# Performance work log

Measured on AMD Instinct MI355X. Metric: run time of the kernel, lower is better.

## Reference

```python
import jax, jax.numpy as jnp
import numpy as np

N_IN, M_MID = 512, 256
B, H, W = 16, 64, 64

def setup_inputs() -> dict:
    key = jax.random.key(0)
    ks = jax.random.split(key, 7)
    s = 0.05
    return {
        "x": jax.random.normal(ks[0], (B, N_IN, H, W), dtype=jnp.float32),
        "W_state": jax.random.normal(ks[1], (M_MID, N_IN), dtype=jnp.float32) * s,
        "b_state": jax.random.normal(ks[2], (M_MID,), dtype=jnp.float32) * s,
        "W_proj": jax.random.normal(ks[3], (M_MID, N_IN), dtype=jnp.float32) * s,
        "b_proj": jax.random.normal(ks[4], (M_MID,), dtype=jnp.float32) * s,
        "W_extend": jax.random.normal(ks[5], (N_IN, M_MID), dtype=jnp.float32) * s,
        "b_extend": jax.random.normal(ks[6], (N_IN,), dtype=jnp.float32) * s,
    }

def reference(x, W_state, b_state, W_proj, b_proj, W_extend, b_extend):
    n, c, h, w = x.shape
    hw = h * w
    xf = x.reshape(n, c, hw)                                   # [n, C, HW]
    # 1x1 convs are channel GEMMs over flattened spatial dim
    x_state = jnp.einsum('mc,nch->nmh', W_state, xf) + b_state[None, :, None]   # [n, M, HW]
    x_proj = jnp.einsum('mc,nch->nmh', W_proj, xf) + b_proj[None, :, None]      # [n, M, HW]
    # bmm -> scale -> softmax -> bmm (graph reasoning over M x M)
    scores = jnp.einsum('nmh,nkh->nmk', x_state, x_proj) / jnp.sqrt(jnp.float32(hw))
    attn = jax.nn.softmax(scores, axis=2)                      # [n, M, M]
    x_rstate = jnp.einsum('nmk,nkh->nmh', attn, x_proj)        # [n, M, HW]
    # extend back to C channels + residual
    ext = jnp.einsum('cm,nmh->nch', W_extend, x_rstate) + b_extend[None, :, None]
    return x + ext.reshape(n, c, h, w)
```

## Files before the change

### kernel.cpp

```cpp
#include <hip/hip_runtime.h>
#include <hip/hip_bf16.h>
#include <stdint.h>

typedef __bf16 bf16x8_t __attribute__((ext_vector_type(8)));
typedef float  f32x4_t  __attribute__((ext_vector_type(4)));
typedef short  short8_t __attribute__((ext_vector_type(8)));

__device__ __forceinline__ unsigned short f2b(float f) {
    union { float f; unsigned u; } v; v.f = f;
    unsigned u = v.u;
    return (unsigned short)((u + 0x7FFFu + ((u >> 16) & 1u)) >> 16);
}
__device__ __forceinline__ float b2f(unsigned short b) {
    union { unsigned u; float f; } v; v.u = ((unsigned)b) << 16; return v.f;
}

#define AS3(p) ((__attribute__((address_space(3))) void*)(p))
#define AS1(p) ((const __attribute__((address_space(1))) void*)(p))
#define FENCE() asm volatile("" ::: "memory")

#define NB   16
#define CIN  512
#define MMID 256
#define HW   4096
#define KSPLIT 4
#define ASZ  (128 * 64)
#define ASZA (512 * 64)
#define ASZB (128 * 64)

__device__ __forceinline__ void swz3(int gx, int gy, int& bx, int& by, int& bz) {
    const int nwg = gridDim.x, ord = blockIdx.x, q = nwg >> 3;
    const int s = (ord & 7) * q + (ord >> 3);
    by = s % gy;
    const int rem = s / gy;
    bx = rem % gx;
    bz = rem / gx;
}

__global__ __launch_bounds__(256) void prep_weights(
    const float* __restrict__ Ws, const float* __restrict__ Wp,
    const float* __restrict__ Wef, const float* __restrict__ bs,
    const float* __restrict__ bp,
    unsigned short* __restrict__ Wsp, unsigned short* __restrict__ Wex,
    unsigned short* __restrict__ WpT, float* __restrict__ bsp)
{
    int i = blockIdx.x * 256 + threadIdx.x;
    if (i < MMID * CIN) {
        Wsp[i]              = f2b(Ws[i]);
        Wsp[MMID * CIN + i] = f2b(Wp[i]);
        Wex[i]              = f2b(Wef[i]);
        const int c = i >> 8, k = i & (MMID - 1);
        WpT[i] = f2b(Wp[(size_t)k * CIN + c]);
    }
    if (i < MMID) { bsp[i] = bs[i]; bsp[MMID + i] = bp[i]; }
}

__global__ __launch_bounds__(256) void transpose_convert_x(
    const float* __restrict__ x, unsigned short* __restrict__ xT)
{
    __shared__ unsigned short tile[64][66];
    const int n = blockIdx.z, c0 = blockIdx.y * 64, h0 = blockIdx.x * 64;
    const float* s = x + ((size_t)n * CIN + c0) * HW + h0;
    unsigned short* d = xT + ((size_t)n * HW + h0) * CIN + c0;
    const int t = threadIdx.x;
    {
        const int rr = t >> 4, cc = (t & 15) * 4;
        #pragma unroll
        for (int p = 0; p < 4; ++p) {
            int r = p * 16 + rr;
            float4 v = *(const float4*)(s + (size_t)r * HW + cc);
            tile[r][cc + 0] = f2b(v.x); tile[r][cc + 1] = f2b(v.y);
            tile[r][cc + 2] = f2b(v.z); tile[r][cc + 3] = f2b(v.w);
        }
    }
    __syncthreads();
    {
        const int wr = t >> 3, wc = (t & 7) * 8;
        #pragma unroll
        for (int p = 0; p < 2; ++p) {
            int h = p * 32 + wr;
            unsigned short tmp[8];
            #pragma unroll
            for (int j = 0; j < 8; ++j) tmp[j] = tile[wc + j][h];
            *(short8_t*)(d + (size_t)h * CIN + wc) = *(const short8_t*)tmp;
        }
    }
}

__global__ __launch_bounds__(256) void transpose_bf16_64(
    const unsigned short* __restrict__ src, unsigned short* __restrict__ dst,
    int srs, int drs, long long sbs, long long dbs)
{
    __shared__ unsigned short tile[64][66];
    const int n = blockIdx.z, r0 = blockIdx.y * 64, c0 = blockIdx.x * 64;
    const unsigned short* s = src + (size_t)n * sbs + (size_t)r0 * srs + c0;
    unsigned short* d = dst + (size_t)n * dbs + (size_t)c0 * drs + r0;
    const int t = threadIdx.x;
    const int rr = t >> 3, cc = (t & 7) * 8;
    #pragma unroll
    for (int p = 0; p < 2; ++p) {
        int r = p * 32 + rr;
        short8_t v = *(const short8_t*)(s + (size_t)r * srs + cc);
        #pragma unroll
        for (int j = 0; j < 8; ++j) tile[r][cc + j] = ((const unsigned short*)&v)[j];
    }
    __syncthreads();
    #pragma unroll
    for (int p = 0; p < 2; ++p) {
        int c = p * 32 + rr;
        unsigned short tmp[8];
        #pragma unroll
        for (int j = 0; j < 8; ++j) tmp[j] = tile[cc + j][c];
        *(short8_t*)(d + (size_t)c * drs + cc) = *(const short8_t*)tmp;
    }
}

template <int EPI>
__device__ __forceinline__ void epilogue_repack(
    f32x4_t (&acc)[4][4], unsigned short* smem,
    int m0, int n0, int wave, int lane,
    void* __restrict__ Cout, int ldc, size_t cbase)
{
    float* fbuf = (float*)smem;
    const int t   = wave * 64 + lane;
    const int l15 = lane & 15, l16 = lane >> 4;
    const int wr2 = wave >> 1;
    const int wc  = (wave & 1) * 64;

    #pragma unroll
    for (int p = 0; p < 4; ++p) {
        __syncthreads();
        if (wr2 == (p >> 1)) {
            const int ihalf = p & 1;
            #pragma unroll
            for (int i2 = 0; i2 < 2; ++i2) {
                const int i = ihalf * 2 + i2;
                #pragma unroll
                for (int r = 0; r < 4; ++r) {
                    const int lrow = i2 * 16 + l16 * 4 + r;
                    #pragma unroll
                    for (int j = 0; j < 4; ++j)
                        fbuf[lrow * 132 + wc + j * 16 + l15] = acc[i][j][r];
                }
            }
        }
        __syncthreads();
        #pragma unroll
        for (int it = 0; it < 2; ++it) {
            const int lrow = it * 16 + (t >> 4);
            const int col  = (t & 15) * 8;
            const int row  = m0 + p * 32 + lrow;
            float v[8];
            *(float4*)&v[0] = *(const float4*)&fbuf[lrow * 132 + col];
            *(float4*)&v[4] = *(const float4*)&fbuf[lrow * 132 + col + 4];
            const size_t idx = cbase + (size_t)row * ldc + n0 + col;
            if constexpr (EPI == 1) {
                float* op = (float*)Cout + idx;
                *(float4*)op = *(const float4*)&v[0];
                *(float4*)(op + 4) = *(const float4*)&v[4];
            } else if constexpr (EPI == 4) {
                unsigned short o[8];
                #pragma unroll
                for (int k = 0; k < 8; ++k)
                    o[k] = f2b(v[k] + ((row == n0 + col + k) ? 1.0f : 0.0f));
                *(short8_t*)((unsigned short*)Cout + idx) = *(const short8_t*)o;
            } else {
                unsigned short o[8];
                #pragma unroll
                for (int k = 0; k < 8; ++k) o[k] = f2b(v[k]);
                *(short8_t*)((unsigned short*)Cout + idx) = *(const short8_t*)o;
            }
        }
    }
}

#define GEMM_KLOOP(Ab, Bb, lda, ldb, KBEG, NT)                                          \
    auto stage = [&](int k0, int b) {                                                   \
        unsigned short* Asb = smem + b * 2 * ASZ;                                       \
        unsigned short* Bsb = Asb + ASZ;                                                \
        _Pragma("unroll")                                                               \
        for (int c = 0; c < 4; ++c) {                                                   \
            const int o   = (c * 256 + t) * 16;                                         \
            const int row = o >> 7;                                                     \
            const int ce  = ((o & 127) ^ ((row & 7) << 4)) >> 1;                        \
            __builtin_amdgcn_global_load_lds(                                           \
                AS1(Ab + (size_t)row * lda + k0 + ce), AS3((char*)Asb + o), 16, 0, 0);  \
            __builtin_amdgcn_global_load_lds(                                           \
                AS1(Bb + (size_t)row * ldb + k0 + ce), AS3((char*)Bsb + o), 16, 0, 0);  \
        }                                                                               \
    };                                                                                  \
    stage(KBEG, 0);                                                                     \
    for (int itk = 0; itk < (NT); ++itk) {                                              \
        const int cur = itk & 1;                                                        \
        if (itk + 1 < (NT)) {                                                           \
            stage(KBEG + (itk + 1) * 64, cur ^ 1);                                      \
            asm volatile("s_waitcnt vmcnt(8)" ::: "memory");                            \
        } else {                                                                        \
            asm volatile("s_waitcnt vmcnt(0)" ::: "memory");                            \
        }                                                                               \
        __builtin_amdgcn_s_barrier();                                                   \
        FENCE();                                                                        \
        const char* Asb = (const char*)(smem + cur * 2 * ASZ);                          \
        const char* Bsb = Asb + 2 * ASZ;                                                \
        const int swz = (l15 & 7) << 4;                                                 \
        _Pragma("unroll")                                                               \
        for (int ks = 0; ks < 2; ++ks) {                                                \
            bf16x8_t af[4], bfr[4];                                                     \
            const int cb = (ks * 64 + l16 * 16) ^ swz;                                  \
            _Pragma("unroll")                                                           \
            for (int i = 0; i < 4; ++i) {                                               \
                af[i]  = *(const bf16x8_t*)(Asb + (wr + i * 16 + l15) * 128 + cb);      \
                bfr[i] = *(const bf16x8_t*)(Bsb + (wc + i * 16 + l15) * 128 + cb);      \
            }                                                                           \
            _Pragma("unroll")                                                           \
            for (int i = 0; i < 4; ++i)                                                 \
                _Pragma("unroll")                                                       \
                for (int j = 0; j < 4; ++j)                                             \
                    acc[i][j] = __builtin_amdgcn_mfma_f32_16x16x32_bf16(                \
                        af[i], bfr[j], acc[i][j], 0, 0, 0);                             \
        }                                                                               \
        FENCE();                                                                        \
        __builtin_amdgcn_s_barrier();                                                   \
        FENCE();                                                                        \
    }

template <int EPI>
__global__ __launch_bounds__(512, 1) void gemm512(
    const unsigned short* __restrict__ A, const unsigned short* __restrict__ B,
    long long strideA, long long strideB,
    const float* __restrict__ bias, int bias_bstride,
    void* __restrict__ Cout, int ldc, long long strideC, int gx)
{
    __shared__ unsigned short smem[2 * (ASZA + ASZB)];

    int bx, by, n;  swz3(gx, 1, bx, by, n);
    const int n0 = bx * 128;

    const unsigned short* Ab = A + (size_t)n * strideA;
    const unsigned short* Bb = B + (size_t)n * strideB + (size_t)n0 * CIN;

    const int t    = threadIdx.x;
    const int lane = t & 63;
    const int wave = t >> 6;
    const int wr   = (wave >> 1) * 128;
    const int wc   = (wave & 1) * 64;
    const int l15  = lane & 15;
    const int l16  = lane >> 4;

    f32x4_t acc[8][4] = {};

    auto stage = [&](int k0, int b) {
        unsigned short* Asb = smem + b * (ASZA + ASZB);
        unsigned short* Bsb = Asb + ASZA;
        #pragma unroll
        for (int c = 0; c < 8; ++c) {
            const int o   = (c * 512 + t) * 16;
            const int row = o >> 7;
            const int ce  = ((o & 127) ^ ((row & 7) << 4)) >> 1;
            __builtin_amdgcn_global_load_lds(
                AS1(Ab + (size_t)row * CIN + k0 + ce), AS3((char*)Asb + o), 16, 0, 0);
        }
        #pragma unroll
        for (int c = 0; c < 2; ++c) {
            const int o   = (c * 512 + t) * 16;
            const int row = o >> 7;
            const int ce  = ((o & 127) ^ ((row & 7) << 4)) >> 1;
            __builtin_amdgcn_global_load_lds(
                AS1(Bb + (size_t)row * CIN + k0 + ce), AS3((char*)Bsb + o), 16, 0, 0);
        }
    };

    const int NT = CIN / 64;
    stage(0, 0);
    for (int itk = 0; itk < NT; ++itk) {
        const int cur = itk & 1;
        if (itk + 1 < NT) {
            stage((itk + 1) * 64, cur ^ 1);
            asm volatile("s_waitcnt vmcnt(10)" ::: "memory");
        } else {
            asm volatile("s_waitcnt vmcnt(0)" ::: "memory");
        }
        __builtin_amdgcn_s_barrier();
        FENCE();
        const char* Asb = (const char*)(smem + cur * (ASZA + ASZB));
        const char* Bsb = Asb + 2 * ASZA;
        const int swz = (l15 & 7) << 4;
        #pragma unroll
        for (int ks = 0; ks < 2; ++ks) {
            const int cb = (ks * 64 + l16 * 16) ^ swz;
            bf16x8_t af[8], bfr[4];
            #pragma unroll
            for (int i = 0; i < 8; ++i)
                af[i] = *(const bf16x8_t*)(Asb + (wr + i * 16 + l15) * 128 + cb);
            #pragma unroll
            for (int j = 0; j < 4; ++j)
                bfr[j] = *(const bf16x8_t*)(Bsb + (wc + j * 16 + l15) * 128 + cb);
            #pragma unroll
            for (int i = 0; i < 8; ++i)
                #pragma unroll
                for (int j = 0; j < 4; ++j)
                    acc[i][j] = __builtin_amdgcn_mfma_f32_16x16x32_bf16(
                        af[i], bfr[j], acc[i][j], 0, 0, 0);
        }
        FENCE();
        __builtin_amdgcn_s_barrier();
        FENCE();
    }

    float* fbuf = (float*)smem;
    const size_t cbase = (size_t)n * strideC;
    const float* beff = bias + (size_t)n * bias_bstride;
    #pragma unroll
    for (int p = 0; p < 16; ++p) {
        __syncthreads();
        if ((wave >> 1) == (p >> 2)) {
            #pragma unroll
            for (int i2 = 0; i2 < 2; ++i2) {
                const int i = (p & 3) * 2 + i2;
                #pragma unroll
                for (int r = 0; r < 4; ++r) {
                    const int lrow = i2 * 16 + l16 * 4 + r;
                    #pragma unroll
                    for (int j = 0; j < 4; ++j)
                        fbuf[lrow * 132 + wc + j * 16 + l15] = acc[i][j][r];
                }
            }
        }
        __syncthreads();
        const int lrow = t >> 4;
        const int col  = (t & 15) * 8;
        const int row  = p * 32 + lrow;
        float v[8];
        *(float4*)&v[0] = *(const float4*)&fbuf[lrow * 132 + col];
        *(float4*)&v[4] = *(const float4*)&fbuf[lrow * 132 + col + 4];
        const float badd = beff[row];
        const size_t idx = cbase + (size_t)row * ldc + n0 + col;
        if constexpr (EPI == 1) {
            float o[8];
            #pragma unroll
            for (int k = 0; k < 8; ++k) o[k] = v[k] + badd;
            float* op = (float*)Cout + idx;
            *(float4*)op = *(const float4*)&o[0];
            *(float4*)(op + 4) = *(const float4*)&o[4];
        } else {
            unsigned short o[8];
            #pragma unroll
            for (int k = 0; k < 8; ++k) o[k] = f2b(v[k] + badd);
            *(short8_t*)((unsigned short*)Cout + idx) = *(const short8_t*)o;
        }
    }
}

__global__ __launch_bounds__(256) void gemm_scores(
    const unsigned short* __restrict__ Ysp, float* __restrict__ scoresP)
{
    __shared__ unsigned short smem[4 * ASZ];

    int bx, by, z;  swz3(MMID / 128, MMID / 128, bx, by, z);
    const int n  = z >> 2;
    const int kc = z & 3;
    const int m0 = by * 128;
    const int n0 = bx * 128;

    const unsigned short* Ab = Ysp + (size_t)n * CIN * HW + (size_t)m0 * HW;
    const unsigned short* Bb = Ysp + (size_t)n * CIN * HW + (size_t)(MMID + n0) * HW;

    const int t    = threadIdx.x;
    const int lane = t & 63;
    const int wave = t >> 6;
    const int wr   = (wave >> 1) * 64;
    const int wc   = (wave & 1) * 64;
    const int l15  = lane & 15;
    const int l16  = lane >> 4;

    f32x4_t acc[4][4] = {};
    const int kbeg = kc * (HW / KSPLIT);
    GEMM_KLOOP(Ab, Bb, HW, HW, kbeg, (HW / KSPLIT) / 64)

    float* outp = scoresP + (size_t)(kc * NB + n) * MMID * MMID;
    epilogue_repack<1>(acc, smem, m0, n0, wave, lane, outp, MMID, 0);
}

__global__ __launch_bounds__(256) void softmax_rows(
    const float* __restrict__ scoresP, unsigned short* __restrict__ attn)
{
    const int wave = threadIdx.x >> 6;
    const int l    = threadIdx.x & 63;
    const size_t row = (size_t)blockIdx.x * 4 + wave;
    const size_t pstride = (size_t)NB * MMID * MMID;
    float4 v = {0.f, 0.f, 0.f, 0.f};
    #pragma unroll
    for (int p = 0; p < KSPLIT; ++p) {
        float4 u = *(const float4*)(scoresP + p * pstride + row * MMID + l * 4);
        v.x += u.x; v.y += u.y; v.z += u.z; v.w += u.w;
    }
    float mx = fmaxf(fmaxf(v.x, v.y), fmaxf(v.z, v.w));
    #pragma unroll
    for (int off = 32; off; off >>= 1) mx = fmaxf(mx, __shfl_xor(mx, off));
    const float sc = 0.015625f;
    float e0 = __expf((v.x - mx) * sc), e1 = __expf((v.y - mx) * sc);
    float e2 = __expf((v.z - mx) * sc), e3 = __expf((v.w - mx) * sc);
    float sum = e0 + e1 + e2 + e3;
    #pragma unroll
    for (int off = 32; off; off >>= 1) sum += __shfl_xor(sum, off);
    const float inv = 1.0f / sum;
    unsigned short o[4] = { f2b(e0 * inv), f2b(e1 * inv), f2b(e2 * inv), f2b(e3 * inv) };
    *(uint64_t*)(attn + row * MMID + l * 4) = *(const uint64_t*)o;
}

__global__ __launch_bounds__(256) void compute_vec(
    const unsigned short* __restrict__ G, const float* __restrict__ bsp,
    const float* __restrict__ be, float* __restrict__ vec)
{
    const int n = blockIdx.x >> 1;
    const int c = ((blockIdx.x & 1) << 8) + threadIdx.x;
    const unsigned short* g = G + ((size_t)n * CIN + c) * MMID;
    float s = 0.f;
    for (int k = 0; k < MMID; k += 8) {
        short8_t v = *(const short8_t*)(g + k);
        #pragma unroll
        for (int j = 0; j < 8; ++j)
            s += b2f((unsigned short)v[j]) * bsp[MMID + k + j];
    }
    vec[n * CIN + c] = be[c] + s;
}

template <int EPI>
__global__ __launch_bounds__(256) void gemm_nt(
    const unsigned short* __restrict__ A, const unsigned short* __restrict__ B,
    int lda, int ldb, int K,
    long long strideA, long long strideB,
    void* __restrict__ Cout, int ldc, long long strideC,
    int gx, int gy)
{
    __shared__ unsigned short smem[4 * ASZ];

    int bx, by, n;  swz3(gx, gy, bx, by, n);
    const int m0 = by * 128;
    const int n0 = bx * 128;

    const unsigned short* Ab = A + (size_t)n * strideA + (size_t)m0 * lda;
    const unsigned short* Bb = B + (size_t)n * strideB + (size_t)n0 * ldb;

    const int t    = threadIdx.x;
    const int lane = t & 63;
    const int wave = t >> 6;
    const int wr   = (wave >> 1) * 64;
    const int wc   = (wave & 1) * 64;
    const int l15  = lane & 15;
    const int l16  = lane >> 4;

    f32x4_t acc[4][4] = {};
    GEMM_KLOOP(Ab, Bb, lda, ldb, 0, K / 64)

    epilogue_repack<EPI>(acc, smem, m0, n0, wave, lane,
                         Cout, ldc, (size_t)n * strideC);
}

extern "C" void kernel_launch(void* const* d_in, const int* in_sizes, int n_in,
                              void* d_out, int out_size, void* d_ws, size_t ws_size,
                              hipStream_t stream)
{
    const float* x   = (const float*)d_in[0];
    const float* Ws  = (const float*)d_in[1];
    const float* bs  = (const float*)d_in[2];
    const float* Wp  = (const float*)d_in[3];
    const float* bp  = (const float*)d_in[4];
    const float* Wef = (const float*)d_in[5];
    const float* be  = (const float*)d_in[6];
    float* out = (float*)d_out;

    unsigned short* xT   = (unsigned short*)d_ws;
    unsigned short* Ysp  = xT   + (size_t)NB * HW * CIN;
    unsigned short* Wsp  = Ysp  + (size_t)NB * CIN * HW;
    unsigned short* Wex  = Wsp  + (size_t)CIN * CIN;
    unsigned short* WpT  = Wex  + (size_t)CIN * MMID;
    unsigned short* attn = WpT  + (size_t)CIN * MMID;
    unsigned short* attnT= attn + (size_t)NB * MMID * MMID;
    unsigned short* G    = attnT+ (size_t)NB * MMID * MMID;
    unsigned short* Meff = G    + (size_t)NB * CIN * MMID;
    float* scoresP = (float*)(Meff + (size_t)NB * CIN * CIN);
    float* bsp = scoresP + (size_t)KSPLIT * NB * MMID * MMID;
    float* vec = bsp + CIN;

    prep_weights<<<512, 256, 0, stream>>>(Ws, Wp, Wef, bs, bp, Wsp, Wex, WpT, bsp);

    transpose_convert_x<<<dim3(HW / 64, CIN / 64, NB), 256, 0, stream>>>(x, xT);

    gemm512<0><<<(HW / 128) * NB, 512, 0, stream>>>(
        Wsp, xT, 0LL, (long long)HW * CIN,
        bsp, 0, Ysp, HW, (long long)CIN * HW, HW / 128);

    gemm_scores<<<(MMID / 128) * (MMID / 128) * NB * KSPLIT, 256, 0, stream>>>(
        Ysp, scoresP);

    softmax_rows<<<NB * MMID / 4, 256, 0, stream>>>(scoresP, attn);

    transpose_bf16_64<<<dim3(MMID / 64, MMID / 64, NB), 256, 0, stream>>>(
        attn, attnT, MMID, MMID, (long long)MMID * MMID, (long long)MMID * MMID);

    gemm_nt<2><<<(MMID / 128) * (CIN / 128) * NB, 256, 0, stream>>>(
        Wex, attnT, MMID, MMID, MMID,
        0LL, (long long)MMID * MMID,
        G, MMID, (long long)CIN * MMID,
        MMID / 128, CIN / 128);

    compute_vec<<<NB * 2, 256, 0, stream>>>(G, bsp, be, vec);

    gemm_nt<4><<<(CIN / 128) * (CIN / 128) * NB, 256, 0, stream>>>(
        G, WpT, MMID, MMID, MMID,
        (long long)CIN * MMID, 0LL,
        Meff, CIN, (long long)CIN * CIN,
        CIN / 128, CIN / 128);

    gemm512<1><<<(HW / 128) * NB, 512, 0, stream>>>(
        Meff, xT, (long long)CIN * CIN, (long long)HW * CIN,
        vec, CIN, out, HW, (long long)CIN * HW, HW / 128);
}
```

Measured before the change: 206.4 us.

## Replace 512x128 single-occupancy GEMM with 256x64 tiles at two blocks per CU

The two big channel GEMMs move from 512-thread blocks computing 512x128 output tiles (one block per CU) to 256-thread blocks computing 256x64 tiles with launch bounds that allow two blocks per CU. Each wave now holds a 64x64 accumulator instead of 128x64, which frees registers and halves LDS use per block so two blocks can share a CU and overlap loads with MFMA work. The cost is lower arithmetic intensity per tile: the B tile is smaller relative to A, so global and LDS traffic per FLOP goes up. Grid size grows fourfold.

```diff
diff --git a/kernel.cpp b/kernel.cpp
--- a/kernel.cpp
+++ b/kernel.cpp
@@ -25,8 +25,8 @@
 #define HW   4096
 #define KSPLIT 4
 #define ASZ  (128 * 64)
-#define ASZA (512 * 64)
-#define ASZB (128 * 64)
+#define ASZA3 (256 * 64)
+#define ASZB3 (64 * 64)
 
 __device__ __forceinline__ void swz3(int gx, int gy, int& bx, int& by, int& bz) {
     const int nwg = gridDim.x, ord = blockIdx.x, q = nwg >> 3;
@@ -225,36 +225,37 @@
     }
 
 template <int EPI>
-__global__ __launch_bounds__(512, 1) void gemm512(
+__global__ __launch_bounds__(256, 2) void gemm_occ2(
     const unsigned short* __restrict__ A, const unsigned short* __restrict__ B,
     long long strideA, long long strideB,
     const float* __restrict__ bias, int bias_bstride,
-    void* __restrict__ Cout, int ldc, long long strideC, int gx)
-{
-    __shared__ unsigned short smem[2 * (ASZA + ASZB)];
-
-    int bx, by, n;  swz3(gx, 1, bx, by, n);
-    const int n0 = bx * 128;
-
-    const unsigned short* Ab = A + (size_t)n * strideA;
+    void* __restrict__ Cout, int ldc, long long strideC,
+    int gx, int gy)
+{
+    __shared__ unsigned short smem[2 * (ASZA3 + ASZB3)];
+
+    int bx, by, n;  swz3(gx, gy, bx, by, n);
+    const int m0 = by * 256;
+    const int n0 = bx * 64;
+
+    const unsigned short* Ab = A + (size_t)n * strideA + (size_t)m0 * CIN;
     const unsigned short* Bb = B + (size_t)n * strideB + (size_t)n0 * CIN;
 
     const int t    = threadIdx.x;
     const int lane = t & 63;
     const int wave = t >> 6;
-    const int wr   = (wave >> 1) * 128;
-    const int wc   = (wave & 1) * 64;
+    const int wr   = wave * 64;
     const int l15  = lane & 15;
     const int l16  = lane >> 4;
 
-    f32x4_t acc[8][4] = {};
+    f32x4_t acc[4][4] = {};
 
     auto stage = [&](int k0, int b) {
-        unsigned short* Asb = smem + b * (ASZA + ASZB);
-        unsigned short* Bsb = Asb + ASZA;
+        unsigned short* Asb = smem + b * (ASZA3 + ASZB3);
+        unsigned short* Bsb = Asb + ASZA3;
         #pragma unroll
         for (int c = 0; c < 8; ++c) {
-            const int o   = (c * 512 + t) * 16;
+            const int o   = (c * 256 + t) * 16;
             const int row = o >> 7;
             const int ce  = ((o & 127) ^ ((row & 7) << 4)) >> 1;
             __builtin_amdgcn_global_load_lds(
@@ -262,7 +263,7 @@
         }
         #pragma unroll
         for (int c = 0; c < 2; ++c) {
-            const int o   = (c * 512 + t) * 16;
+            const int o   = (c * 256 + t) * 16;
             const int row = o >> 7;
             const int ce  = ((o & 127) ^ ((row & 7) << 4)) >> 1;
             __builtin_amdgcn_global_load_lds(
@@ -282,21 +283,21 @@
         }
         __builtin_amdgcn_s_barrier();
         FENCE();
-        const char* Asb = (const char*)(smem + cur * (ASZA + ASZB));
-        const char* Bsb = Asb + 2 * ASZA;
+        const char* Asb = (const char*)(smem + cur * (ASZA3 + ASZB3));
+        const char* Bsb = Asb + 2 * ASZA3;
         const int swz = (l15 & 7) << 4;
         #pragma unroll
         for (int ks = 0; ks < 2; ++ks) {
             const int cb = (ks * 64 + l16 * 16) ^ swz;
-            bf16x8_t af[8], bfr[4];
-            #pragma unroll
-            for (int i = 0; i < 8; ++i)
+            bf16x8_t af[4], bfr[4];
+            #pragma unroll
+            for (int i = 0; i < 4; ++i)
                 af[i] = *(const bf16x8_t*)(Asb + (wr + i * 16 + l15) * 128 + cb);
             #pragma unroll
             for (int j = 0; j < 4; ++j)
-                bfr[j] = *(const bf16x8_t*)(Bsb + (wc + j * 16 + l15) * 128 + cb);
-            #pragma unroll
-            for (int i = 0; i < 8; ++i)
+                bfr[j] = *(const bf16x8_t*)(Bsb + (j * 16 + l15) * 128 + cb);
+            #pragma unroll
+            for (int i = 0; i < 4; ++i)
                 #pragma unroll
                 for (int j = 0; j < 4; ++j)
                     acc[i][j] = __builtin_amdgcn_mfma_f32_16x16x32_bf16(
@@ -311,28 +312,28 @@
     const size_t cbase = (size_t)n * strideC;
     const float* beff = bias + (size_t)n * bias_bstride;
     #pragma unroll
-    for (int p = 0; p < 16; ++p) {
+    for (int p = 0; p < 8; ++p) {
         __syncthreads();
-        if ((wave >> 1) == (p >> 2)) {
+        if (wave == (p >> 1)) {
             #pragma unroll
             for (int i2 = 0; i2 < 2; ++i2) {
-                const int i = (p & 3) * 2 + i2;
+                const int i = (p & 1) * 2 + i2;
                 #pragma unroll
                 for (int r = 0; r < 4; ++r) {
                     const int lrow = i2 * 16 + l16 * 4 + r;
                     #pragma unroll
                     for (int j = 0; j < 4; ++j)
-                        fbuf[lrow * 132 + wc + j * 16 + l15] = acc[i][j][r];
+                        fbuf[lrow * 68 + j * 16 + l15] = acc[i][j][r];
                 }
             }
         }
         __syncthreads();
-        const int lrow = t >> 4;
-        const int col  = (t & 15) * 8;
-        const int row  = p * 32 + lrow;
+        const int lrow = t >> 3;
+        const int col  = (t & 7) * 8;
+        const int row  = m0 + p * 32 + lrow;
         float v[8];
-        *(float4*)&v[0] = *(const float4*)&fbuf[lrow * 132 + col];
-        *(float4*)&v[4] = *(const float4*)&fbuf[lrow * 132 + col + 4];
+        *(float4*)&v[0] = *(const float4*)&fbuf[lrow * 68 + col];
+        *(float4*)&v[4] = *(const float4*)&fbuf[lrow * 68 + col + 4];
         const float badd = beff[row];
         const size_t idx = cbase + (size_t)row * ldc + n0 + col;
         if constexpr (EPI == 1) {
@@ -487,9 +488,10 @@
 
     transpose_convert_x<<<dim3(HW / 64, CIN / 64, NB), 256, 0, stream>>>(x, xT);
 
-    gemm512<0><<<(HW / 128) * NB, 512, 0, stream>>>(
+    gemm_occ2<0><<<(CIN / 256) * (HW / 64) * NB, 256, 0, stream>>>(
         Wsp, xT, 0LL, (long long)HW * CIN,
-        bsp, 0, Ysp, HW, (long long)CIN * HW, HW / 128);
+        bsp, 0, Ysp, HW, (long long)CIN * HW,
+        HW / 64, CIN / 256);
 
     gemm_scores<<<(MMID / 128) * (MMID / 128) * NB * KSPLIT, 256, 0, stream>>>(
         Ysp, scoresP);
@@ -513,7 +515,8 @@
         Meff, CIN, (long long)CIN * CIN,
         CIN / 128, CIN / 128);
 
-    gemm512<1><<<(HW / 128) * NB, 512, 0, stream>>>(
+    gemm_occ2<1><<<(CIN / 256) * (HW / 64) * NB, 256, 0, stream>>>(
         Meff, xT, (long long)CIN * CIN, (long long)HW * CIN,
-        vec, CIN, out, HW, (long long)CIN * HW, HW / 128);
-}
+        vec, CIN, out, HW, (long long)CIN * HW,
+        HW / 64, CIN / 256);
+}
```

Result: faster. 197.4 us (median of 3 runs) (-4.3%).
